# Optimization experiments

Hardware: AMD Instinct MI355X
Metric: run time of the kernel (lower is better)

The kernel has to match this reference:

```python
import jax, jax.numpy as jnp
import numpy as np

ALPHA = 0.5      # GCN2Conv alpha
THETA = 1.0      # GCN2Conv theta (beta_l = log(theta/l + 1))
EPS = 1e-5       # pyg LayerNorm eps
N_LAYERS = 8
N, E, DIN, DHID, DOUT = 50000, 800000, 128, 256, 128


def setup_inputs() -> dict:
    key = jax.random.key(0)
    ks = jax.random.split(key, 10)
    x = jax.random.normal(ks[0], (N, DIN), jnp.float32)
    edge_index = jax.random.randint(ks[1], (2, E), 0, N, dtype=jnp.int32)
    lin1_w = jax.random.normal(ks[2], (DIN, DHID), jnp.float32) / np.sqrt(DIN)
    lin1_b = jnp.zeros((DHID,), jnp.float32)
    conv_w1 = jax.random.normal(ks[3], (N_LAYERS, DHID, DHID), jnp.float32) / np.sqrt(DHID)
    conv_w2 = jax.random.normal(ks[4], (N_LAYERS, DHID, DHID), jnp.float32) / np.sqrt(DHID)
    norm_gamma = jnp.ones((N_LAYERS, DHID), jnp.float32)
    norm_beta = jnp.zeros((N_LAYERS, DHID), jnp.float32)
    lin2_w = jax.random.normal(ks[5], (DHID, DOUT), jnp.float32) / np.sqrt(DHID)
    lin2_b = jnp.zeros((DOUT,), jnp.float32)
    return {"x": x, "edge_index": edge_index, "lin1_w": lin1_w, "lin1_b": lin1_b,
            "conv_w1": conv_w1, "conv_w2": conv_w2, "norm_gamma": norm_gamma,
            "norm_beta": norm_beta, "lin2_w": lin2_w, "lin2_b": lin2_b}


def _gcn_norm(edge_index, n_nodes, dtype):
    # add self loops, then symmetric deg^{-1/2} A_hat deg^{-1/2} normalization
    loop = jnp.arange(n_nodes, dtype=edge_index.dtype)
    row = jnp.concatenate([edge_index[0], loop])
    col = jnp.concatenate([edge_index[1], loop])
    deg = jax.ops.segment_sum(jnp.ones_like(row, dtype=dtype), col, num_segments=n_nodes)
    dis = jnp.where(deg > 0, jax.lax.rsqrt(jnp.maximum(deg, 1e-12)), 0.0)
    return row, col, dis[row] * dis[col]


def _graph_layernorm(h, gamma, beta):
    # pyg LayerNorm mode='graph', batch=None: normalize over all nodes+features
    z = h - jnp.mean(h)
    z = z / (jnp.sqrt(jnp.mean(z * z)) + EPS)
    return gamma * z + beta


def reference(x, edge_index, lin1_w, lin1_b, conv_w1, conv_w2, norm_gamma, norm_beta, lin2_w, lin2_b):
    n_nodes = x.shape[0]
    row, col, enorm = _gcn_norm(edge_index, n_nodes, x.dtype)
    # lin1 + relu (dropout p=0 -> identity); residual=None -> zeros
    x0 = jax.nn.relu(x @ lin1_w + lin1_b)
    h = x0
    for i in range(conv_w1.shape[0]):
        beta_l = float(np.log(THETA / (i + 1) + 1.0))
        # sparse neighborhood aggregation: out[c] += norm * h[r]
        agg = jax.ops.segment_sum(h[row] * enorm[:, None], col, num_segments=n_nodes)
        t = (1.0 - ALPHA) * agg          # propagated part
        r = ALPHA * x0                   # initial-residual part (res = x0 + zeros)
        # shared_weights=False: separate weights for propagated and residual parts
        h = (1.0 - beta_l) * (t + r) + beta_l * (t @ conv_w1[i] + r @ conv_w2[i])
        h = jax.nn.relu(_graph_layernorm(h, norm_gamma[i], norm_beta[i]))
    return jax.nn.relu(h @ lin2_w + lin2_b)
```

## Files before the change

kernel.cpp:

```cpp
#include <hip/hip_runtime.h>
#include <hip/hip_bf16.h>
#include <math.h>

#define DIN 128
#define DH 256
#define DOUT 128
#define NLAYERS 8
#define EPSLN 1e-5f

typedef __hip_bfloat16 bf16;
typedef __attribute__((ext_vector_type(8))) short short8;
typedef __attribute__((ext_vector_type(4))) float f32x4;

__device__ __forceinline__ float ldf(const void* p, size_t idx, int isbf) {
    if (isbf) return __bfloat162float(((const bf16*)p)[idx]);
    return ((const float*)p)[idx];
}
__device__ __forceinline__ short f2s(float v) {
    bf16 b = __float2bfloat16(v);
    return *reinterpret_cast<short*>(&b);
}
__device__ __forceinline__ float s2f(short s) {
    unsigned int u = ((unsigned int)(unsigned short)s) << 16;
    float f;
    __builtin_memcpy(&f, &u, 4);
    return f;
}
__device__ __forceinline__ void gl_lds16(const void* g, void* l) {
    __builtin_amdgcn_global_load_lds(
        (const __attribute__((address_space(1))) unsigned int*)g,
        (__attribute__((address_space(3))) unsigned int*)l,
        16, 0, 0);
}

__global__ void k_detect(const unsigned int* __restrict__ xw, int* __restrict__ flag) {
    __shared__ int cnt;
    if (threadIdx.x == 0) cnt = 0;
    __syncthreads();
    unsigned int w = xw[threadIdx.x];
    int e = (w >> 7) & 0xFF;
    if (e >= 112 && e <= 140) atomicAdd(&cnt, 1);
    __syncthreads();
    if (threadIdx.x == 0) *flag = (cnt >= 128) ? 1 : 0;
}

__global__ void k_init_cnt(int* __restrict__ cnt, int N) {
    int i = blockIdx.x * blockDim.x + threadIdx.x;
    if (i < N) cnt[i] = 0;
}
__global__ void k_count(const int* __restrict__ cols, int* __restrict__ cnt, int E) {
    int e = blockIdx.x * blockDim.x + threadIdx.x;
    if (e < E) atomicAdd(&cnt[cols[e]], 1);
}
__global__ void k_dis(const int* __restrict__ cnt, float* __restrict__ dis, int N) {
    int i = blockIdx.x * blockDim.x + threadIdx.x;
    if (i < N) dis[i] = rsqrtf(1.0f + (float)cnt[i]);
}
__global__ void k_scan1(const int* __restrict__ cnt, int* __restrict__ rowptr,
                        int* __restrict__ bsum, int N) {
    __shared__ int s[256];
    int t = threadIdx.x;
    int i = blockIdx.x * 256 + t;
    s[t] = (i < N) ? cnt[i] : 0;
    __syncthreads();
    for (int off = 1; off < 256; off <<= 1) {
        int x = (t >= off) ? s[t - off] : 0;
        __syncthreads();
        s[t] += x;
        __syncthreads();
    }
    if (i < N) rowptr[i + 1] = s[t];
    if (t == 255) bsum[blockIdx.x] = s[255];
}
__global__ void k_scan2(int* __restrict__ bsum, int nb) {
    __shared__ int s[256];
    int t = threadIdx.x;
    s[t] = (t < nb) ? bsum[t] : 0;
    __syncthreads();
    for (int off = 1; off < 256; off <<= 1) {
        int x = (t >= off) ? s[t - off] : 0;
        __syncthreads();
        s[t] += x;
        __syncthreads();
    }
    if (t < nb) bsum[t] = s[t];
}
__global__ void k_scan3(int* __restrict__ rowptr, const int* __restrict__ bsum, int N) {
    int i = blockIdx.x * 256 + threadIdx.x;
    if (i == 0) rowptr[0] = 0;
    if (i < N && blockIdx.x > 0) rowptr[i + 1] += bsum[blockIdx.x - 1];
}
__global__ void k_cursor(const int* __restrict__ rowptr, int* __restrict__ cursor, int N) {
    int i = blockIdx.x * 256 + threadIdx.x;
    if (i < N) cursor[i] = rowptr[i];
}
__global__ void k_fill(const int* __restrict__ rows, const int* __restrict__ cols,
                       int* __restrict__ cursor, int* __restrict__ csr, int E) {
    int e = blockIdx.x * blockDim.x + threadIdx.x;
    if (e < E) {
        int c = cols[e], r = rows[e];
        int pos = atomicAdd(&cursor[c], 1);
        csr[pos] = r;
    }
}

__global__ void k_zero_stats(float* __restrict__ stats) {
    int t = threadIdx.x;
    if (t < 16) stats[t] = 0.0f;
}

__global__ void k_transw2(const void* __restrict__ w1, const void* __restrict__ w2,
                          const int* __restrict__ flag, short* __restrict__ wt) {
    __shared__ float tile[32][33];
    int z = blockIdx.z;
    int lay = z >> 1, m = z & 1;
    const void* src = m ? w2 : w1;
    size_t sbase = (size_t)lay * 65536;
    short* dst = wt + (size_t)lay * 131072 + (size_t)m * 256;
    float bl = logf(1.0f / (float)(lay + 1) + 1.0f);
    float c0 = 0.5f * (1.0f - bl);
    float c1 = 0.5f * bl;
    int isbf = *flag;
    int tx = threadIdx.x, ty = threadIdx.y;
    int n0 = blockIdx.x * 32, k0 = blockIdx.y * 32;
    #pragma unroll
    for (int i = 0; i < 4; i++) {
        int k = k0 + ty + i * 8;
        tile[ty + i * 8][tx] = ldf(src, sbase + (size_t)k * 256 + n0 + tx, isbf);
    }
    __syncthreads();
    #pragma unroll
    for (int i = 0; i < 4; i++) {
        int n = n0 + ty + i * 8;
        int k = k0 + tx;
        float v = c1 * tile[tx][ty + i * 8];
        if (k == n) v += c0;
        dst[(size_t)n * 512 + k] = f2s(v);
    }
}

__global__ void k_transw_lin(const void* __restrict__ src, const int* __restrict__ flag,
                             short* __restrict__ dst, int K, int Nc) {
    __shared__ float tile[32][33];
    int isbf = *flag;
    int tx = threadIdx.x, ty = threadIdx.y;
    int n0 = blockIdx.x * 32, k0 = blockIdx.y * 32;
    #pragma unroll
    for (int i = 0; i < 4; i++) {
        int k = k0 + ty + i * 8;
        tile[ty + i * 8][tx] = ldf(src, (size_t)k * Nc + n0 + tx, isbf);
    }
    __syncthreads();
    #pragma unroll
    for (int i = 0; i < 4; i++) {
        int n = n0 + ty + i * 8;
        dst[(size_t)n * K + k0 + tx] = f2s(tile[tx][ty + i * 8]);
    }
}

__global__ void k_convx(const void* __restrict__ x, const int* __restrict__ flag,
                        short* __restrict__ xb, int total) {
    int i = blockIdx.x * 256 + threadIdx.x;
    if (i < total) xb[i] = f2s(ldf(x, i, *flag));
}

template<int KK, int FINAL>
__global__ __launch_bounds__(256) void gemm_mfma(
    const short* __restrict__ A, const short* __restrict__ wt,
    const void* __restrict__ bias, const int* __restrict__ flag,
    void* __restrict__ outp, int Nn)
{
    __shared__ __align__(16) short Atile[128 * 32];
    __shared__ __align__(16) short Btile[128 * 32];
    int t = threadIdx.x;
    int w = t >> 6, lane = t & 63;
    int lr = lane & 15, quad = lane >> 4;
    int row0 = blockIdx.x * 128;
    int col0 = blockIdx.y * 128;
    int ncols = gridDim.y * 128;
    int sub = t & 3;
    int srow = t >> 2;
    f32x4 acc[2][8];
    #pragma unroll
    for (int m = 0; m < 2; m++)
        #pragma unroll
        for (int nt = 0; nt < 8; nt++)
            #pragma unroll
            for (int j = 0; j < 4; j++) acc[m][nt][j] = 0.f;

    for (int kb = 0; kb < KK; kb += 32) {
        #pragma unroll
        for (int r = 0; r < 2; r++) {
            int gr = row0 + srow + r * 64;
            if (gr >= Nn) gr = Nn - 1;
            gl_lds16(A + (size_t)gr * KK + kb + sub * 8,
                     Atile + (size_t)(t + r * 256) * 8);
        }
        #pragma unroll
        for (int r = 0; r < 2; r++) {
            int n = col0 + srow + r * 64;
            gl_lds16(wt + (size_t)n * KK + kb + sub * 8,
                     Btile + (size_t)(t + r * 256) * 8);
        }
        __syncthreads();
        short8 a0 = *(const short8*)(Atile + (w * 32 + lr) * 32 + quad * 8);
        short8 a1 = *(const short8*)(Atile + (w * 32 + 16 + lr) * 32 + quad * 8);
        #pragma unroll
        for (int nt = 0; nt < 8; nt++) {
            short8 bv = *(const short8*)(Btile + (nt * 16 + lr) * 32 + quad * 8);
            acc[0][nt] = __builtin_amdgcn_mfma_f32_16x16x32_bf16(a0, bv, acc[0][nt], 0, 0, 0);
            acc[1][nt] = __builtin_amdgcn_mfma_f32_16x16x32_bf16(a1, bv, acc[1][nt], 0, 0, 0);
        }
        __syncthreads();
    }
    const int isbf = *flag;
    #pragma unroll
    for (int m = 0; m < 2; m++) {
        #pragma unroll
        for (int nt = 0; nt < 8; nt++) {
            int gc = col0 + nt * 16 + lr;
            float bb = ldf(bias, gc, isbf);
            #pragma unroll
            for (int i = 0; i < 4; i++) {
                int gr = row0 + w * 32 + m * 16 + quad * 4 + i;
                if (gr < Nn) {
                    float v = acc[m][nt][i] + bb;
                    v = v > 0.f ? v : 0.f;
                    size_t off = (size_t)gr * ncols + gc;
                    if (FINAL) {
                        if (isbf) ((bf16*)outp)[off] = __float2bfloat16(v);
                        else      ((float*)outp)[off] = v;
                    } else {
                        ((bf16*)outp)[off] = __float2bfloat16(v);
                    }
                }
            }
        }
    }
}

__global__ __launch_bounds__(256) void k_gather3(
    const int* __restrict__ rowptr, const int* __restrict__ csr,
    const float* __restrict__ dis, const bf16* __restrict__ hsrc,
    bf16* __restrict__ agg,
    const void* __restrict__ g, const void* __restrict__ b, size_t loff,
    const float* __restrict__ stats2, float invTotal, int useLN,
    const int* __restrict__ flag, int N)
{
    int t = threadIdx.x;
    int wave = t >> 6, lane = t & 63;
    int half = lane >> 5;
    int sl = lane & 31;
    int node = blockIdx.x * 8 + wave * 2 + half;
    bool ok = node < N;
    if (!ok) node = N - 1;
    int col = sl * 8;
    float cA[8], cB[8];
    if (useLN) {
        int isbf = *flag;
        float mu = stats2[0] * invTotal;
        float var = stats2[1] * invTotal - mu * mu;
        var = var > 0.f ? var : 0.f;
        float inv = 1.0f / (sqrtf(var) + EPSLN);
        #pragma unroll
        for (int j = 0; j < 8; j++) {
            float gg = ldf(g, loff + col + j, isbf);
            float bb = ldf(b, loff + col + j, isbf);
            cA[j] = gg * inv;
            cB[j] = fmaf(-gg * inv, mu, bb);
        }
    } else {
        #pragma unroll
        for (int j = 0; j < 8; j++) { cA[j] = 1.0f; cB[j] = 0.0f; }
    }
    const short* hs = (const short*)hsrc;
    float dc = dis[node];
    float acc[8];
    {
        short8 hv = *(const short8*)(hs + (size_t)node * DH + col);
        #pragma unroll
        for (int j = 0; j < 8; j++) {
            float v = fmaf(cA[j], s2f(hv[j]), cB[j]);
            v = v > 0.f ? v : 0.f;
            acc[j] = dc * v;
        }
    }
    int i = rowptr[node], e1 = rowptr[node + 1];
    for (; i + 2 <= e1; i += 2) {
        int r0 = csr[i], r1 = csr[i + 1];
        float w0 = dis[r0], w1 = dis[r1];
        short8 v0 = *(const short8*)(hs + (size_t)r0 * DH + col);
        short8 v1 = *(const short8*)(hs + (size_t)r1 * DH + col);
        #pragma unroll
        for (int j = 0; j < 8; j++) {
            float a0 = fmaf(cA[j], s2f(v0[j]), cB[j]); a0 = a0 > 0.f ? a0 : 0.f;
            float a1 = fmaf(cA[j], s2f(v1[j]), cB[j]); a1 = a1 > 0.f ? a1 : 0.f;
            acc[j] = fmaf(w0, a0, acc[j]);
            acc[j] = fmaf(w1, a1, acc[j]);
        }
    }
    for (; i < e1; i++) {
        int r = csr[i];
        float wr = dis[r];
        short8 v0 = *(const short8*)(hs + (size_t)r * DH + col);
        #pragma unroll
        for (int j = 0; j < 8; j++) {
            float a0 = fmaf(cA[j], s2f(v0[j]), cB[j]); a0 = a0 > 0.f ? a0 : 0.f;
            acc[j] = fmaf(wr, a0, acc[j]);
        }
    }
    if (ok) {
        short8 o;
        #pragma unroll
        for (int j = 0; j < 8; j++) o[j] = f2s(dc * acc[j]);
        *(short8*)((short*)agg + (size_t)node * DH + col) = o;
    }
}

__global__ __launch_bounds__(256) void gemm_layer4(
    const bf16* __restrict__ agg, const bf16* __restrict__ x0,
    const short* __restrict__ wt, bf16* __restrict__ h,
    float* __restrict__ stats2, int Nn)
{
    __shared__ __align__(16) short Atile[128 * 32];
    __shared__ __align__(16) short Btile[128 * 32];
    __shared__ float red[512];
    int t = threadIdx.x;
    int w = t >> 6, lane = t & 63;
    int lr = lane & 15, quad = lane >> 4;
    int row0 = blockIdx.x * 128;
    int col0 = blockIdx.y * 128;
    int sub = t & 3;
    int srow = t >> 2;
    f32x4 acc[2][8];
    #pragma unroll
    for (int m = 0; m < 2; m++)
        #pragma unroll
        for (int nt = 0; nt < 8; nt++)
            #pragma unroll
            for (int j = 0; j < 4; j++) acc[m][nt][j] = 0.f;

    for (int kb = 0; kb < 512; kb += 32) {
        const short* Asrc = (const short*)((kb < DH) ? agg : x0);
        int ka = kb & (DH - 1);
        #pragma unroll
        for (int r = 0; r < 2; r++) {
            int gr = row0 + srow + r * 64;
            if (gr >= Nn) gr = Nn - 1;
            gl_lds16(Asrc + (size_t)gr * DH + ka + sub * 8,
                     Atile + (size_t)(t + r * 256) * 8);
        }
        #pragma unroll
        for (int r = 0; r < 2; r++) {
            int n = col0 + srow + r * 64;
            gl_lds16(wt + (size_t)n * 512 + kb + sub * 8,
                     Btile + (size_t)(t + r * 256) * 8);
        }
        __syncthreads();
        short8 a0 = *(const short8*)(Atile + (w * 32 + lr) * 32 + quad * 8);
        short8 a1 = *(const short8*)(Atile + (w * 32 + 16 + lr) * 32 + quad * 8);
        #pragma unroll
        for (int nt = 0; nt < 8; nt++) {
            short8 bv = *(const short8*)(Btile + (nt * 16 + lr) * 32 + quad * 8);
            acc[0][nt] = __builtin_amdgcn_mfma_f32_16x16x32_bf16(a0, bv, acc[0][nt], 0, 0, 0);
            acc[1][nt] = __builtin_amdgcn_mfma_f32_16x16x32_bf16(a1, bv, acc[1][nt], 0, 0, 0);
        }
        __syncthreads();
    }
    float lsum = 0.f, lsq = 0.f;
    #pragma unroll
    for (int m = 0; m < 2; m++) {
        #pragma unroll
        for (int nt = 0; nt < 8; nt++) {
            int gc = col0 + nt * 16 + lr;
            #pragma unroll
            for (int i = 0; i < 4; i++) {
                int gr = row0 + w * 32 + m * 16 + quad * 4 + i;
                if (gr < Nn) {
                    float v = acc[m][nt][i];
                    h[(size_t)gr * DH + gc] = __float2bfloat16(v);
                    lsum += v;
                    lsq += v * v;
                }
            }
        }
    }
    red[t] = lsum;
    red[256 + t] = lsq;
    __syncthreads();
    for (int s = 128; s > 0; s >>= 1) {
        if (t < s) { red[t] += red[t + s]; red[256 + t] += red[256 + t + s]; }
        __syncthreads();
    }
    if (t == 0) {
        atomicAdd(&stats2[0], red[0]);
        atomicAdd(&stats2[1], red[256]);
    }
}

__global__ __launch_bounds__(256) void k_applyT(
    bf16* __restrict__ h, const float* __restrict__ stats2, float invTotal,
    const void* __restrict__ g, const void* __restrict__ b, size_t loff,
    const int* __restrict__ flag, int total)
{
    int idx = blockIdx.x * 256 + threadIdx.x;
    if (idx >= total) return;
    const int isbf = *flag;
    float mu = stats2[0] * invTotal;
    float var = stats2[1] * invTotal - mu * mu;
    var = var > 0.f ? var : 0.f;
    float inv = 1.0f / (sqrtf(var) + EPSLN);
    int j = idx & (DH - 1);
    float gg = ldf(g, loff + j, isbf);
    float bb = ldf(b, loff + j, isbf);
    float v = fmaf(gg * inv, __bfloat162float(h[idx]), fmaf(-gg * inv, mu, bb));
    v = v > 0.f ? v : 0.f;
    h[idx] = __float2bfloat16(v);
}

extern "C" void kernel_launch(void* const* d_in, const int* in_sizes, int n_in,
                              void* d_out, int out_size, void* d_ws, size_t ws_size,
                              hipStream_t stream) {
    const void* x      = d_in[0];
    const int*  ei     = (const int*)d_in[1];
    const void* lin1_w = d_in[2];
    const void* lin1_b = d_in[3];
    const void* conv_w1= d_in[4];
    const void* conv_w2= d_in[5];
    const void* gam    = d_in[6];
    const void* bet    = d_in[7];
    const void* lin2_w = d_in[8];
    const void* lin2_b = d_in[9];

    const int N = in_sizes[0] / DIN;
    const int E = in_sizes[1] / 2;
    const int* rows = ei;
    const int* cols = ei + E;
    const size_t NDH = (size_t)N * DH;
    const size_t Nr = ((size_t)N + 255) / 256 * 256;

    char* p = (char*)d_ws;
    auto alloc = [&](size_t bytes) { char* q = p; p += (bytes + 255) & ~(size_t)255; return q; };
    float* dis    = (float*)alloc(Nr * 4);
    float* stats  = (float*)alloc(1024);
    int*   flag   = (int*)(stats + 16);
    int*   cnt    = (int*)alloc(Nr * 4);
    int*   rowptr = (int*)alloc((Nr + 256) * 4);
    int*   cursor = (int*)alloc(Nr * 4);
    int*   bsum   = (int*)alloc(1024);
    int*   csr    = (int*)alloc((size_t)E * 4);
    short* wt     = (short*)alloc((size_t)NLAYERS * 131072 * 2);
    short* w1t    = (short*)alloc((size_t)DH * DIN * 2);
    short* w2t    = (short*)alloc((size_t)DOUT * DH * 2);
    short* xb     = (short*)alloc((size_t)N * DIN * 2);
    bf16*  agg    = (bf16*)alloc(NDH * 2);
    bf16*  x0     = (bf16*)alloc(NDH * 2);
    bf16*  h      = (bf16*)alloc(NDH * 2);

    dim3 blk(256);
    int nbN = (N + 255) / 256;
    dim3 gN(nbN);
    dim3 gE((E + 255) / 256);
    dim3 gB128_2((N + 127) / 128, 2);
    dim3 gB128_1((N + 127) / 128, 1);
    dim3 gG((N + 7) / 8);
    dim3 gElem((unsigned)((NDH + 255) / 256));
    dim3 gTW(8, 8, 16);
    dim3 bTW(32, 8);

    k_detect<<<1, 256, 0, stream>>>((const unsigned int*)x, flag);
    k_init_cnt<<<gN, blk, 0, stream>>>(cnt, N);
    k_count<<<gE, blk, 0, stream>>>(cols, cnt, E);
    k_dis<<<gN, blk, 0, stream>>>(cnt, dis, N);
    k_scan1<<<gN, blk, 0, stream>>>(cnt, rowptr, bsum, N);
    k_scan2<<<1, 256, 0, stream>>>(bsum, nbN);
    k_scan3<<<gN, blk, 0, stream>>>(rowptr, bsum, N);
    k_cursor<<<gN, blk, 0, stream>>>(rowptr, cursor, N);
    k_fill<<<gE, blk, 0, stream>>>(rows, cols, cursor, csr, E);
    k_zero_stats<<<1, 64, 0, stream>>>(stats);
    k_transw2<<<gTW, bTW, 0, stream>>>(conv_w1, conv_w2, flag, wt);
    k_transw_lin<<<dim3(DH / 32, DIN / 32), bTW, 0, stream>>>(lin1_w, flag, w1t, DIN, DH);
    k_transw_lin<<<dim3(DOUT / 32, DH / 32), bTW, 0, stream>>>(lin2_w, flag, w2t, DH, DOUT);
    k_convx<<<dim3((unsigned)(((size_t)N * DIN + 255) / 256)), blk, 0, stream>>>(x, flag, xb, N * DIN);

    gemm_mfma<DIN, 0><<<gB128_2, blk, 0, stream>>>(xb, w1t, lin1_b, flag, x0, N);

    const float invTotal = 1.0f / ((float)N * (float)DH);
    for (int l = 0; l < NLAYERS; l++) {
        const bf16* hsrc = (l == 0) ? x0 : h;
        size_t loff = (l == 0) ? 0 : (size_t)(l - 1) * DH;
        const float* st = (l == 0) ? stats : stats + 2 * (l - 1);
        k_gather3<<<gG, blk, 0, stream>>>(rowptr, csr, dis, hsrc, agg,
                                          gam, bet, loff, st, invTotal,
                                          l > 0 ? 1 : 0, flag, N);
        gemm_layer4<<<gB128_2, blk, 0, stream>>>(agg, x0, wt + (size_t)l * 131072,
                                                 h, stats + 2 * l, N);
    }
    k_applyT<<<gElem, blk, 0, stream>>>(h, stats + 2 * (NLAYERS - 1), invTotal,
                                        gam, bet, (size_t)(NLAYERS - 1) * DH,
                                        flag, (int)NDH);
    gemm_mfma<DH, 1><<<gB128_1, blk, 0, stream>>>((const short*)h, w2t, lin2_b,
                                                  flag, d_out, N);
}
```

Before: 1.339 ms.

## Unfuse layernorm from gather, apply it in place before a lighter gather

Moves the graph layernorm+ReLU out of the sparse gather into a separate elementwise k_applyT pass over h before each layer. The gather then only does a weighted sum of raw bf16 rows, with 8-way unrolled independent loads and four accumulators. It also drops from 8 to 4 columns per thread, so each node gets a full 64-lane wave. This removes per-edge normalization ALU work and raises memory-level parallelism, at the cost of an extra full read+write of h per layer.

```diff
diff --git a/kernel.cpp b/kernel.cpp
--- a/kernel.cpp
+++ b/kernel.cpp
@@ -10,6 +10,7 @@
 
 typedef __hip_bfloat16 bf16;
 typedef __attribute__((ext_vector_type(8))) short short8;
+typedef __attribute__((ext_vector_type(4))) short short4v;
 typedef __attribute__((ext_vector_type(4))) float f32x4;
 
 __device__ __forceinline__ float ldf(const void* p, size_t idx, int isbf) {
@@ -239,82 +240,74 @@
     }
 }
 
-__global__ __launch_bounds__(256) void k_gather3(
+__global__ __launch_bounds__(256) void k_gather4(
     const int* __restrict__ rowptr, const int* __restrict__ csr,
     const float* __restrict__ dis, const bf16* __restrict__ hsrc,
-    bf16* __restrict__ agg,
-    const void* __restrict__ g, const void* __restrict__ b, size_t loff,
-    const float* __restrict__ stats2, float invTotal, int useLN,
-    const int* __restrict__ flag, int N)
+    bf16* __restrict__ agg, int N)
 {
-    int t = threadIdx.x;
-    int wave = t >> 6, lane = t & 63;
-    int half = lane >> 5;
-    int sl = lane & 31;
-    int node = blockIdx.x * 8 + wave * 2 + half;
-    bool ok = node < N;
-    if (!ok) node = N - 1;
-    int col = sl * 8;
-    float cA[8], cB[8];
-    if (useLN) {
-        int isbf = *flag;
-        float mu = stats2[0] * invTotal;
-        float var = stats2[1] * invTotal - mu * mu;
-        var = var > 0.f ? var : 0.f;
-        float inv = 1.0f / (sqrtf(var) + EPSLN);
-        #pragma unroll
-        for (int j = 0; j < 8; j++) {
-            float gg = ldf(g, loff + col + j, isbf);
-            float bb = ldf(b, loff + col + j, isbf);
-            cA[j] = gg * inv;
-            cB[j] = fmaf(-gg * inv, mu, bb);
-        }
-    } else {
-        #pragma unroll
-        for (int j = 0; j < 8; j++) { cA[j] = 1.0f; cB[j] = 0.0f; }
-    }
+    int gid = blockIdx.x * 256 + threadIdx.x;
+    int node = gid >> 6;
+    if (node >= N) return;
+    int col = (gid & 63) * 4;
     const short* hs = (const short*)hsrc;
     float dc = dis[node];
-    float acc[8];
+    float a0[4], a1[4], a2[4], a3[4];
     {
-        short8 hv = *(const short8*)(hs + (size_t)node * DH + col);
-        #pragma unroll
-        for (int j = 0; j < 8; j++) {
-            float v = fmaf(cA[j], s2f(hv[j]), cB[j]);
-            v = v > 0.f ? v : 0.f;
-            acc[j] = dc * v;
+        short4v hv = *(const short4v*)(hs + (size_t)node * DH + col);
+        #pragma unroll
+        for (int j = 0; j < 4; j++) {
+            a0[j] = dc * s2f(hv[j]);
+            a1[j] = 0.f; a2[j] = 0.f; a3[j] = 0.f;
         }
     }
     int i = rowptr[node], e1 = rowptr[node + 1];
+    for (; i + 8 <= e1; i += 8) {
+        int r0 = csr[i],     r1 = csr[i + 1], r2 = csr[i + 2], r3 = csr[i + 3];
+        int r4 = csr[i + 4], r5 = csr[i + 5], r6 = csr[i + 6], r7 = csr[i + 7];
+        float w0 = dis[r0], w1 = dis[r1], w2 = dis[r2], w3 = dis[r3];
+        float w4 = dis[r4], w5 = dis[r5], w6 = dis[r6], w7 = dis[r7];
+        short4v v0 = *(const short4v*)(hs + (size_t)r0 * DH + col);
+        short4v v1 = *(const short4v*)(hs + (size_t)r1 * DH + col);
+        short4v v2 = *(const short4v*)(hs + (size_t)r2 * DH + col);
+        short4v v3 = *(const short4v*)(hs + (size_t)r3 * DH + col);
+        short4v v4 = *(const short4v*)(hs + (size_t)r4 * DH + col);
+        short4v v5 = *(const short4v*)(hs + (size_t)r5 * DH + col);
+        short4v v6 = *(const short4v*)(hs + (size_t)r6 * DH + col);
+        short4v v7 = *(const short4v*)(hs + (size_t)r7 * DH + col);
+        #pragma unroll
+        for (int j = 0; j < 4; j++) {
+            a0[j] = fmaf(w0, s2f(v0[j]), a0[j]);
+            a1[j] = fmaf(w1, s2f(v1[j]), a1[j]);
+            a2[j] = fmaf(w2, s2f(v2[j]), a2[j]);
+            a3[j] = fmaf(w3, s2f(v3[j]), a3[j]);
+            a0[j] = fmaf(w4, s2f(v4[j]), a0[j]);
+            a1[j] = fmaf(w5, s2f(v5[j]), a1[j]);
+            a2[j] = fmaf(w6, s2f(v6[j]), a2[j]);
+            a3[j] = fmaf(w7, s2f(v7[j]), a3[j]);
+        }
+    }
     for (; i + 2 <= e1; i += 2) {
         int r0 = csr[i], r1 = csr[i + 1];
         float w0 = dis[r0], w1 = dis[r1];
-        short8 v0 = *(const short8*)(hs + (size_t)r0 * DH + col);
-        short8 v1 = *(const short8*)(hs + (size_t)r1 * DH + col);
-        #pragma unroll
-        for (int j = 0; j < 8; j++) {
-            float a0 = fmaf(cA[j], s2f(v0[j]), cB[j]); a0 = a0 > 0.f ? a0 : 0.f;
-            float a1 = fmaf(cA[j], s2f(v1[j]), cB[j]); a1 = a1 > 0.f ? a1 : 0.f;
-            acc[j] = fmaf(w0, a0, acc[j]);
-            acc[j] = fmaf(w1, a1, acc[j]);
+        short4v v0 = *(const short4v*)(hs + (size_t)r0 * DH + col);
+        short4v v1 = *(const short4v*)(hs + (size_t)r1 * DH + col);
+        #pragma unroll
+        for (int j = 0; j < 4; j++) {
+            a0[j] = fmaf(w0, s2f(v0[j]), a0[j]);
+            a1[j] = fmaf(w1, s2f(v1[j]), a1[j]);
         }
     }
     for (; i < e1; i++) {
         int r = csr[i];
         float wr = dis[r];
-        short8 v0 = *(const short8*)(hs + (size_t)r * DH + col);
-        #pragma unroll
-        for (int j = 0; j < 8; j++) {
-            float a0 = fmaf(cA[j], s2f(v0[j]), cB[j]); a0 = a0 > 0.f ? a0 : 0.f;
-            acc[j] = fmaf(wr, a0, acc[j]);
-        }
-    }
-    if (ok) {
-        short8 o;
-        #pragma unroll
-        for (int j = 0; j < 8; j++) o[j] = f2s(dc * acc[j]);
-        *(short8*)((short*)agg + (size_t)node * DH + col) = o;
-    }
+        short4v v0 = *(const short4v*)(hs + (size_t)r * DH + col);
+        #pragma unroll
+        for (int j = 0; j < 4; j++) a0[j] = fmaf(wr, s2f(v0[j]), a0[j]);
+    }
+    short4v o;
+    #pragma unroll
+    for (int j = 0; j < 4; j++) o[j] = f2s(dc * ((a0[j] + a1[j]) + (a2[j] + a3[j])));
+    *(short4v*)((short*)agg + (size_t)node * DH + col) = o;
 }
 
 __global__ __launch_bounds__(256) void gemm_layer4(
@@ -463,7 +456,7 @@
     dim3 gE((E + 255) / 256);
     dim3 gB128_2((N + 127) / 128, 2);
     dim3 gB128_1((N + 127) / 128, 1);
-    dim3 gG((N + 7) / 8);
+    dim3 gG((N + 3) / 4);
     dim3 gElem((unsigned)((NDH + 255) / 256));
     dim3 gTW(8, 8, 16);
     dim3 bTW(32, 8);
@@ -488,11 +481,12 @@
     const float invTotal = 1.0f / ((float)N * (float)DH);
     for (int l = 0; l < NLAYERS; l++) {
         const bf16* hsrc = (l == 0) ? x0 : h;
-        size_t loff = (l == 0) ? 0 : (size_t)(l - 1) * DH;
-        const float* st = (l == 0) ? stats : stats + 2 * (l - 1);
-        k_gather3<<<gG, blk, 0, stream>>>(rowptr, csr, dis, hsrc, agg,
-                                          gam, bet, loff, st, invTotal,
-                                          l > 0 ? 1 : 0, flag, N);
+        if (l > 0) {
+            k_applyT<<<gElem, blk, 0, stream>>>(h, stats + 2 * (l - 1), invTotal,
+                                                gam, bet, (size_t)(l - 1) * DH,
+                                                flag, (int)NDH);
+        }
+        k_gather4<<<gG, blk, 0, stream>>>(rowptr, csr, dis, hsrc, agg, N);
         gemm_layer4<<<gB128_2, blk, 0, stream>>>(agg, x0, wt + (size_t)l * 131072,
                                                  h, stats + 2 * l, N);
     }
```

Result: no change. 1.329 ms (-0.7%).
